# Optimization experiments

Measured on AMD Instinct MI355X. Metric: run time of the kernel, lower is better.

The kernel has to match this reference:

```python
import jax, jax.numpy as jnp
from jax import lax
import numpy as np

B, T, I, H = 4096, 200, 32, 6  # batch, seq_len, input_size, hidden


def _lstm_layer(x_seq, W_ih, W_hh, b_ih, b_hh):
    """Single unidirectional LSTM layer, PyTorch gate order (i,f,g,o).
    x_seq: [B,T,Din]. Returns (all_h [B,T,H], h_last [B,H])."""
    Bb = x_seq.shape[0]
    Hh = W_hh.shape[1]
    # Precompute input projections for all timesteps (hoisted out of the scan).
    x_proj = jnp.einsum('bti,gi->btg', x_seq, W_ih) + b_ih + b_hh  # [B,T,4H]

    def step(carry, xp_t):
        h, c = carry
        gates = xp_t + h @ W_hh.T  # [B,4H]
        i_g, f_g, g_g, o_g = jnp.split(gates, 4, axis=-1)
        i_g = jax.nn.sigmoid(i_g)
        f_g = jax.nn.sigmoid(f_g)
        g_g = jnp.tanh(g_g)
        o_g = jax.nn.sigmoid(o_g)
        c = f_g * c + i_g * g_g
        h = o_g * jnp.tanh(c)
        return (h, c), h

    init = (jnp.zeros((Bb, Hh), x_seq.dtype), jnp.zeros((Bb, Hh), x_seq.dtype))
    (h_last, _), hs = lax.scan(step, init, jnp.swapaxes(x_proj, 0, 1))  # time-major scan
    return jnp.swapaxes(hs, 0, 1), h_last


def setup_inputs() -> dict:
    key = jax.random.key(0)
    ks = jax.random.split(key, 11)
    s = 0.2  # ~ uniform(-1/sqrt(H)) scale for H=6
    inp = {
        'x': jax.random.normal(ks[0], (B, T, I), dtype=jnp.float32),
        'W_ih0': jax.random.normal(ks[1], (4 * H, I), dtype=jnp.float32) * s,
        'W_hh0': jax.random.normal(ks[2], (4 * H, H), dtype=jnp.float32) * s,
        'b_ih0': jax.random.normal(ks[3], (4 * H,), dtype=jnp.float32) * s,
        'b_hh0': jax.random.normal(ks[4], (4 * H,), dtype=jnp.float32) * s,
        'W_ih1': jax.random.normal(ks[5], (4 * H, H), dtype=jnp.float32) * s,
        'W_hh1': jax.random.normal(ks[6], (4 * H, H), dtype=jnp.float32) * s,
        'b_ih1': jax.random.normal(ks[7], (4 * H,), dtype=jnp.float32) * s,
        'b_hh1': jax.random.normal(ks[8], (4 * H,), dtype=jnp.float32) * s,
        'W_lin': jax.random.normal(ks[9], (1, H), dtype=jnp.float32) * s,
        'b_lin': jax.random.normal(ks[10], (1,), dtype=jnp.float32) * s,
    }
    return inp


def reference(x, W_ih0, W_hh0, b_ih0, b_hh0, W_ih1, W_hh1, b_ih1, b_hh1, W_lin, b_lin):
    # Layer 0 (eval mode: inter-layer dropout disabled)
    h1_seq, _ = _lstm_layer(x, W_ih0, W_hh0, b_ih0, b_hh0)
    # Layer 1
    _, h2_last = _lstm_layer(h1_seq, W_ih1, W_hh1, b_ih1, b_hh1)
    # Linear head on last layer's final hidden state: [B,1]
    return h2_last @ W_lin.T + b_lin
```

## Files before the change

### kernel.cpp

```cpp
#include <hip/hip_runtime.h>


#define BATCH 4096
#define TLEN  200
#define ISZ   32
#define HSZ   6
#define GSZ   24
#define TCH   64
#define XPITCH 28
#define XROWS (TCH + 1)

__device__ __forceinline__ float fast_sig(float x) {
    return __builtin_amdgcn_rcpf(1.0f + __expf(-x));
}
__device__ __forceinline__ float rl(float v, int l) {
    return __int_as_float(__builtin_amdgcn_readlane(__float_as_int(v), l));
}
template <int CTRL>
__device__ __forceinline__ float qperm(float v) {
    return __int_as_float(__builtin_amdgcn_mov_dpp(__float_as_int(v), CTRL, 0xf, 0xf, true));
}

__global__ void __launch_bounds__(64)
lstm_fused(
    const float* __restrict__ x,
    const float* __restrict__ Wih0, const float* __restrict__ Whh0,
    const float* __restrict__ bih0, const float* __restrict__ bhh0,
    const float* __restrict__ Wih1, const float* __restrict__ Whh1,
    const float* __restrict__ bih1, const float* __restrict__ bhh1,
    const float* __restrict__ Wlin, const float* __restrict__ blin,
    float* __restrict__ out)
{
    __shared__ __align__(16) float xp_lds[XROWS * XPITCH];

    const int lane = threadIdx.x;
    const int b    = blockIdx.x;

    const bool loHalf = (lane < 32);
    const int  p  = lane & 3;
    const int  jq = (lane & 31) >> 2;
    const int  j  = (jq < HSZ) ? jq : 0;
    const int  r  = 6 * p + j;

    float WA[HSZ], WB[HSZ];
    float base1 = 0.0f;
#pragma unroll
    for (int k = 0; k < HSZ; ++k) { WA[k] = 0.0f; WB[k] = 0.0f; }
    if (loHalf) {
#pragma unroll
        for (int k = 0; k < HSZ; ++k) WA[k] = Whh0[r * HSZ + k];
    } else {
#pragma unroll
        for (int k = 0; k < HSZ; ++k) { WA[k] = Wih1[r * HSZ + k]; WB[k] = Whh1[r * HSZ + k]; }
        base1 = bih1[r] + bhh1[r];
    }
    const float mg  = (p == 2) ? 2.0f : 1.0f;
    const float sg  = (p == 2) ? 2.0f : 1.0f;
    const float tgc = (p == 2) ? -1.0f : 0.0f;

    float c = 0.0f, h = 0.0f;

    for (int t0 = 0; t0 < TLEN; t0 += TCH) {
        const int tcl = min(TCH, TLEN - t0);

        {
            const int tIdx = min(t0 + lane, TLEN - 1);
            const float4* xrow = (const float4*)(x + ((size_t)b * TLEN + tIdx) * ISZ);
#pragma unroll
            for (int grp = 0; grp < 3; ++grp) {
                float acc[8];
#pragma unroll
                for (int rr = 0; rr < 8; ++rr)
                    acc[rr] = bih0[grp * 8 + rr] + bhh0[grp * 8 + rr];
#pragma unroll
                for (int kh = 0; kh < 2; ++kh) {
                    float4 xr[4];
#pragma unroll
                    for (int q = 0; q < 4; ++q) xr[q] = xrow[4 * kh + q];
#pragma unroll
                    for (int rr = 0; rr < 8; ++rr) {
                        const float4* wrow =
                            (const float4*)(Wih0 + (grp * 8 + rr) * ISZ + kh * 16);
#pragma unroll
                        for (int q = 0; q < 4; ++q) {
                            float4 w = wrow[q];
                            acc[rr] += w.x * xr[q].x + w.y * xr[q].y
                                     + w.z * xr[q].z + w.w * xr[q].w;
                        }
                    }
                }
                *(float4*)&xp_lds[lane * XPITCH + 8 * grp] =
                    make_float4(acc[0], acc[1], acc[2], acc[3]);
                *(float4*)&xp_lds[lane * XPITCH + 8 * grp + 4] =
                    make_float4(acc[4], acc[5], acc[6], acc[7]);
            }
        }

        const bool lastChunk = (t0 + TCH >= TLEN);
        const int  iters = tcl + (lastChunk ? 1 : 0);
        float xp_cur = xp_lds[r];
        int   it0 = 0;

        if (t0 == 0) {
            const float g  = loHalf ? xp_cur : base1;
            const float a  = fmaf(sg, fast_sig(mg * g), tgc);
            const float iq = qperm<0x00>(a);
            const float gq = qperm<0xAA>(a);
            const float oq = qperm<0xFF>(a);
            const float cn = iq * gq;
            const float th = fmaf(2.0f, fast_sig(2.0f * cn), -1.0f);
            const float hn = oq * th;
            c = loHalf ? cn : 0.0f;
            h = loHalf ? hn : 0.0f;
            xp_cur = xp_lds[XPITCH + r];
            it0 = 1;
        }

        for (int it = it0; it < iters; ++it) {
            const float h10 = rl(h, 0),  h11 = rl(h, 4),  h12 = rl(h, 8);
            const float h13 = rl(h, 12), h14 = rl(h, 16), h15 = rl(h, 20);
            const float h20 = rl(h, 32), h21 = rl(h, 36), h22 = rl(h, 40);
            const float h23 = rl(h, 44), h24 = rl(h, 48), h25 = rl(h, 52);

            const float xp_nxt = xp_lds[(it + 1) * XPITCH + r];

            const float g0 = loHalf ? xp_cur : base1;
            float a0 = fmaf(WA[0], h10, fmaf(WA[2], h12, fmaf(WA[4], h14, g0)));
            float a1 = fmaf(WA[1], h11, fmaf(WA[3], h13, WA[5] * h15));
            float b0 = fmaf(WB[0], h20, fmaf(WB[2], h22, WB[4] * h24));
            float b1 = fmaf(WB[1], h21, fmaf(WB[3], h23, WB[5] * h25));
            const float g = (a0 + a1) + (b0 + b1);
            const float a = fmaf(sg, fast_sig(mg * g), tgc);

            const float iq = qperm<0x00>(a);
            const float fq = qperm<0x55>(a);
            const float gq = qperm<0xAA>(a);
            const float oq = qperm<0xFF>(a);

            c = fmaf(fq, c, iq * gq);
            const float th = fmaf(2.0f, fast_sig(2.0f * c), -1.0f);
            h = oq * th;

            xp_cur = xp_nxt;
        }
    }

    float s = blin[0];
#pragma unroll
    for (int k = 0; k < HSZ; ++k) s = fmaf(Wlin[k], rl(h, 32 + 4 * k), s);
    if (lane == 0) out[b] = s;
}

extern "C" void kernel_launch(void* const* d_in, const int* in_sizes, int n_in,
                              void* d_out, int out_size, void* d_ws, size_t ws_size,
                              hipStream_t stream) {
    const float* x    = (const float*)d_in[0];
    const float* Wih0 = (const float*)d_in[1];
    const float* Whh0 = (const float*)d_in[2];
    const float* bih0 = (const float*)d_in[3];
    const float* bhh0 = (const float*)d_in[4];
    const float* Wih1 = (const float*)d_in[5];
    const float* Whh1 = (const float*)d_in[6];
    const float* bih1 = (const float*)d_in[7];
    const float* bhh1 = (const float*)d_in[8];
    const float* Wlin = (const float*)d_in[9];
    const float* blin = (const float*)d_in[10];
    float* out = (float*)d_out;

    lstm_fused<<<BATCH, 64, 0, stream>>>(x, Wih0, Whh0, bih0, bhh0,
                                         Wih1, Whh1, bih1, bhh1,
                                         Wlin, blin, out);
}
```

Measured before the change: 289.9 us.

## Split input projection into separate kernel and stream projections from global memory in scan

Moves the layer-0 input projection out of the fused LSTM kernel into its own grid-parallel kernel that writes a [B,208,24] workspace. The scan kernel then reads the precomputed projections directly from global memory with a two-step register prefetch, instead of computing 64-step chunks into LDS in between recurrent segments. This removes the serialized projection phases from the latency-bound recurrence, but adds a roughly 80 MB workspace round trip, a second launch, and global-load latency inside the scan loop. The old fused kernel is kept as a fallback when the workspace is too small.

```diff
diff --git a/kernel.cpp b/kernel.cpp
--- a/kernel.cpp
+++ b/kernel.cpp
@@ -6,20 +6,150 @@
 #define ISZ   32
 #define HSZ   6
 #define GSZ   24
+#define XPT   208
+#define XPB   (XPT * GSZ)
+
+__device__ __forceinline__ float fast_sig(float x) {
+    return __builtin_amdgcn_rcpf(1.0f + __expf(-x));
+}
+__device__ __forceinline__ float rl(float v, int l) {
+    return __int_as_float(__builtin_amdgcn_readlane(__float_as_int(v), l));
+}
+template <int CTRL>
+__device__ __forceinline__ float qperm(float v) {
+    return __int_as_float(__builtin_amdgcn_mov_dpp(__float_as_int(v), CTRL, 0xf, 0xf, true));
+}
+
+__global__ __launch_bounds__(64) void proj_kernel(
+    const float* __restrict__ x, const float* __restrict__ Wih0,
+    const float* __restrict__ bih0, const float* __restrict__ bhh0,
+    float* __restrict__ xp)
+{
+    const int lane = threadIdx.x;
+    const int t    = blockIdx.x * 64 + lane;
+    const int b    = blockIdx.y;
+    const int tc   = min(t, TLEN - 1);
+    const float4* xrow = (const float4*)(x + ((size_t)b * TLEN + tc) * ISZ);
+    float* orow = xp + (size_t)b * XPB + (size_t)tc * GSZ;
+
+#pragma unroll
+    for (int grp = 0; grp < 3; ++grp) {
+        float acc[8];
+#pragma unroll
+        for (int rr = 0; rr < 8; ++rr) acc[rr] = bih0[grp * 8 + rr] + bhh0[grp * 8 + rr];
+#pragma unroll
+        for (int kh = 0; kh < 2; ++kh) {
+            float4 xr[4];
+#pragma unroll
+            for (int q = 0; q < 4; ++q) xr[q] = xrow[4 * kh + q];
+#pragma unroll
+            for (int rr = 0; rr < 8; ++rr) {
+                const float4* wrow = (const float4*)(Wih0 + (grp * 8 + rr) * ISZ + kh * 16);
+#pragma unroll
+                for (int q = 0; q < 4; ++q) {
+                    float4 w = wrow[q];
+                    acc[rr] += w.x * xr[q].x + w.y * xr[q].y + w.z * xr[q].z + w.w * xr[q].w;
+                }
+            }
+        }
+        if (t < TLEN) {
+            *(float4*)&orow[8 * grp]     = make_float4(acc[0], acc[1], acc[2], acc[3]);
+            *(float4*)&orow[8 * grp + 4] = make_float4(acc[4], acc[5], acc[6], acc[7]);
+        }
+    }
+}
+
+__global__ __launch_bounds__(64) void scan_kernel(
+    const float* __restrict__ xp,
+    const float* __restrict__ Whh0,
+    const float* __restrict__ Wih1, const float* __restrict__ Whh1,
+    const float* __restrict__ bih1, const float* __restrict__ bhh1,
+    const float* __restrict__ Wlin, const float* __restrict__ blin,
+    float* __restrict__ out)
+{
+    const int lane = threadIdx.x;
+    const int b    = blockIdx.x;
+
+    const bool loHalf = (lane < 32);
+    const int  p  = lane & 3;
+    const int  jq = (lane & 31) >> 2;
+    const int  j  = (jq < HSZ) ? jq : 0;
+    const int  r  = 6 * p + j;
+
+    float WA[HSZ], WB[HSZ];
+    float base1 = 0.0f;
+#pragma unroll
+    for (int k = 0; k < HSZ; ++k) { WA[k] = 0.0f; WB[k] = 0.0f; }
+    if (loHalf) {
+#pragma unroll
+        for (int k = 0; k < HSZ; ++k) WA[k] = Whh0[r * HSZ + k];
+    } else {
+#pragma unroll
+        for (int k = 0; k < HSZ; ++k) { WA[k] = Wih1[r * HSZ + k]; WB[k] = Whh1[r * HSZ + k]; }
+        base1 = bih1[r] + bhh1[r];
+    }
+    const float mg  = (p == 2) ? 2.0f : 1.0f;
+    const float sg  = (p == 2) ? 2.0f : 1.0f;
+    const float tgc = (p == 2) ? -1.0f : 0.0f;
+
+    const float* xq = xp + (size_t)b * XPB + r;
+
+    float c = 0.0f, h = 0.0f;
+
+    float x0 = xq[0];
+    float x1 = xq[GSZ];
+    float x2 = xq[2 * GSZ];
+
+    {
+        const float g  = loHalf ? x0 : base1;
+        const float a  = fmaf(sg, fast_sig(mg * g), tgc);
+        const float iq = qperm<0x00>(a);
+        const float gq = qperm<0xAA>(a);
+        const float oq = qperm<0xFF>(a);
+        const float cn = iq * gq;
+        const float th = fmaf(2.0f, fast_sig(2.0f * cn), -1.0f);
+        const float hn = oq * th;
+        c = loHalf ? cn : 0.0f;
+        h = loHalf ? hn : 0.0f;
+    }
+
+    for (int it = 1; it <= TLEN; ++it) {
+        const float h10 = rl(h, 0),  h11 = rl(h, 4),  h12 = rl(h, 8);
+        const float h13 = rl(h, 12), h14 = rl(h, 16), h15 = rl(h, 20);
+        const float h20 = rl(h, 32), h21 = rl(h, 36), h22 = rl(h, 40);
+        const float h23 = rl(h, 44), h24 = rl(h, 48), h25 = rl(h, 52);
+
+        const float xnew = xq[(it + 2) * GSZ];
+
+        const float g0 = loHalf ? x1 : base1;
+        float a0 = fmaf(WA[0], h10, fmaf(WA[2], h12, fmaf(WA[4], h14, g0)));
+        float a1 = fmaf(WA[1], h11, fmaf(WA[3], h13, WA[5] * h15));
+        float b0 = fmaf(WB[0], h20, fmaf(WB[2], h22, WB[4] * h24));
+        float b1 = fmaf(WB[1], h21, fmaf(WB[3], h23, WB[5] * h25));
+        const float g = (a0 + a1) + (b0 + b1);
+        const float a = fmaf(sg, fast_sig(mg * g), tgc);
+
+        const float iq = qperm<0x00>(a);
+        const float fq = qperm<0x55>(a);
+        const float gq = qperm<0xAA>(a);
+        const float oq = qperm<0xFF>(a);
+
+        c = fmaf(fq, c, iq * gq);
+        const float th = fmaf(2.0f, fast_sig(2.0f * c), -1.0f);
+        h = oq * th;
+
+        x1 = x2; x2 = xnew;
+    }
+
+    float s = blin[0];
+#pragma unroll
+    for (int k = 0; k < HSZ; ++k) s = fmaf(Wlin[k], rl(h, 32 + 4 * k), s);
+    if (lane == 0) out[b] = s;
+}
+
 #define TCH   64
 #define XPITCH 28
 #define XROWS (TCH + 1)
-
-__device__ __forceinline__ float fast_sig(float x) {
-    return __builtin_amdgcn_rcpf(1.0f + __expf(-x));
-}
-__device__ __forceinline__ float rl(float v, int l) {
-    return __int_as_float(__builtin_amdgcn_readlane(__float_as_int(v), l));
-}
-template <int CTRL>
-__device__ __forceinline__ float qperm(float v) {
-    return __int_as_float(__builtin_amdgcn_mov_dpp(__float_as_int(v), CTRL, 0xf, 0xf, true));
-}
 
 __global__ void __launch_bounds__(64)
 lstm_fused(
@@ -62,7 +192,6 @@
 
     for (int t0 = 0; t0 < TLEN; t0 += TCH) {
         const int tcl = min(TCH, TLEN - t0);
-
         {
             const int tIdx = min(t0 + lane, TLEN - 1);
             const float4* xrow = (const float4*)(x + ((size_t)b * TLEN + tIdx) * ISZ);
@@ -167,7 +296,15 @@
     const float* blin = (const float*)d_in[10];
     float* out = (float*)d_out;
 
-    lstm_fused<<<BATCH, 64, 0, stream>>>(x, Wih0, Whh0, bih0, bhh0,
-                                         Wih1, Whh1, bih1, bhh1,
-                                         Wlin, blin, out);
-}
+    const size_t need = (size_t)BATCH * XPB * sizeof(float);
+    if (ws_size >= need) {
+        float* xp = (float*)d_ws;
+        proj_kernel<<<dim3(4, BATCH), 64, 0, stream>>>(x, Wih0, bih0, bhh0, xp);
+        scan_kernel<<<BATCH, 64, 0, stream>>>(xp, Whh0, Wih1, Whh1, bih1, bhh1,
+                                              Wlin, blin, out);
+    } else {
+        lstm_fused<<<BATCH, 64, 0, stream>>>(x, Wih0, Whh0, bih0, bhh0,
+                                             Wih1, Whh1, bih1, bhh1,
+                                             Wlin, blin, out);
+    }
+}
```

Result: slower. 336.6 us (+16.1%).

## Interleave layer-0 input projection with recurrent scan using an LDS ring buffer

Applied to the files above, without the earlier changes.

Replaces the chunked scheme, where each 64-step chunk first computed the input projection and then ran the serial recurrence, with a software pipeline. Small slices of the next window's x·W_ih0 projection are computed between scan steps and written into a 64-slot LDS ring. W_ih0 and the biases are staged once in LDS. The gate-g pre-scaling by 2 is folded into the weights, and launch bounds request 4 waves per SIMD. The goal is to hide the projection work in the latency gaps of the serial recurrence, at the cost of more register pressure and more complex indexing.

```diff
diff --git a/kernel.cpp b/kernel.cpp
--- a/kernel.cpp
+++ b/kernel.cpp
@@ -1,14 +1,14 @@
 #include <hip/hip_runtime.h>
 
 
-#define BATCH 4096
 #define TLEN  200
 #define ISZ   32
 #define HSZ   6
-#define GSZ   24
-#define TCH   64
-#define XPITCH 28
-#define XROWS (TCH + 1)
+#define RPITCH 25
+#define RING_DW (64 * RPITCH)
+#define WOFF  RING_DW
+#define BOFF  (WOFF + 768)
+#define LDS_DW (BOFF + 24)
 
 __device__ __forceinline__ float fast_sig(float x) {
     return __builtin_amdgcn_rcpf(1.0f + __expf(-x));
@@ -20,9 +20,11 @@
 __device__ __forceinline__ float qperm(float v) {
     return __int_as_float(__builtin_amdgcn_mov_dpp(__float_as_int(v), CTRL, 0xf, 0xf, true));
 }
-
-__global__ void __launch_bounds__(64)
-lstm_fused(
+__device__ __forceinline__ float dot4(float4 w, float4 v) {
+    return fmaf(w.x, v.x, fmaf(w.y, v.y, fmaf(w.z, v.z, w.w * v.w)));
+}
+
+__global__ __launch_bounds__(64, 4) void lstm_one(
     const float* __restrict__ x,
     const float* __restrict__ Wih0, const float* __restrict__ Whh0,
     const float* __restrict__ bih0, const float* __restrict__ bhh0,
@@ -31,10 +33,13 @@
     const float* __restrict__ Wlin, const float* __restrict__ blin,
     float* __restrict__ out)
 {
-    __shared__ __align__(16) float xp_lds[XROWS * XPITCH];
+    __shared__ float lds[LDS_DW];
 
     const int lane = threadIdx.x;
     const int b    = blockIdx.x;
+
+    const int o = lane & 1;
+    const int L = lane >> 1;
 
     const bool loHalf = (lane < 32);
     const int  p  = lane & 3;
@@ -42,113 +47,175 @@
     const int  j  = (jq < HSZ) ? jq : 0;
     const int  r  = 6 * p + j;
 
-    float WA[HSZ], WB[HSZ];
-    float base1 = 0.0f;
-#pragma unroll
-    for (int k = 0; k < HSZ; ++k) { WA[k] = 0.0f; WB[k] = 0.0f; }
+#define LDSW(ROW, KCQ) (*(const float4*)&lds[WOFF + ((o * 12 + (ROW)) << 5) + ((KCQ) << 2)])
+
+#pragma unroll
+    for (int k = 0; k < 13; ++k) {
+        const int idx = lane + (k << 6);
+        if (idx < 768)      lds[WOFF + idx] = Wih0[idx];
+        else if (idx < 792) lds[BOFF + idx - 768] = bih0[idx - 768] + bhh0[idx - 768];
+    }
+
+    float WA[6], WB[6], base1 = 0.0f, sgc = 1.0f, tgc = 0.0f;
+#pragma unroll
+    for (int k = 0; k < 6; ++k) { WA[k] = 0.0f; WB[k] = 0.0f; }
     if (loHalf) {
 #pragma unroll
-        for (int k = 0; k < HSZ; ++k) WA[k] = Whh0[r * HSZ + k];
+        for (int k = 0; k < 6; ++k) WA[k] = Whh0[r * 6 + k];
     } else {
 #pragma unroll
-        for (int k = 0; k < HSZ; ++k) { WA[k] = Wih1[r * HSZ + k]; WB[k] = Whh1[r * HSZ + k]; }
+        for (int k = 0; k < 6; ++k) { WA[k] = Wih1[r * 6 + k]; WB[k] = Whh1[r * 6 + k]; }
         base1 = bih1[r] + bhh1[r];
     }
-    const float mg  = (p == 2) ? 2.0f : 1.0f;
-    const float sg  = (p == 2) ? 2.0f : 1.0f;
-    const float tgc = (p == 2) ? -1.0f : 0.0f;
+    if (p == 2) {
+#pragma unroll
+        for (int k = 0; k < 6; ++k) { WA[k] *= 2.0f; WB[k] *= 2.0f; }
+        base1 *= 2.0f; sgc = 2.0f; tgc = -1.0f;
+    }
+
+    const float* xb = x + (size_t)b * TLEN * ISZ;
+
+#pragma unroll
+    for (int w01 = 0; w01 < 2; ++w01) {
+        const int t = (w01 << 5) + L;
+        const float4* xr4 = (const float4*)(xb + t * ISZ);
+        float4 xw[8];
+#pragma unroll
+        for (int q = 0; q < 8; ++q) xw[q] = xr4[q];
+        float a0c[12];
+#pragma unroll
+        for (int jj = 0; jj < 12; ++jj) a0c[jj] = 0.0f;
+#pragma unroll
+        for (int kc = 0; kc < 8; ++kc)
+#pragma unroll
+            for (int jj = 0; jj < 12; ++jj)
+                a0c[jj] += dot4(LDSW(jj, kc), xw[kc]);
+#pragma unroll
+        for (int jj = 0; jj < 12; ++jj) {
+            float v = a0c[jj] + lds[BOFF + o * 12 + jj];
+            if (jj < 6) v = (o == 1) ? v * 2.0f : v;
+            lds[t * RPITCH + o * 12 + jj] = v;
+        }
+    }
+
+    float acc[12];
+#pragma unroll
+    for (int jj = 0; jj < 12; ++jj) acc[jj] = 0.0f;
+    const float* pc = xb + (size_t)min(64 + L, TLEN - 1) * ISZ;
+    const float* pn = xb + (size_t)min(96 + L, TLEN - 1) * ISZ;
+    float4 f0, f1;
+    f1 = *((const float4*)pc);
+    float4 Wp0 = LDSW(0, 0), Wp1 = LDSW(1, 0), Wp2 = LDSW(2, 0);
 
     float c = 0.0f, h = 0.0f;
-
-    for (int t0 = 0; t0 < TLEN; t0 += TCH) {
-        const int tcl = min(TCH, TLEN - t0);
-
-        {
-            const int tIdx = min(t0 + lane, TLEN - 1);
-            const float4* xrow = (const float4*)(x + ((size_t)b * TLEN + tIdx) * ISZ);
-#pragma unroll
-            for (int grp = 0; grp < 3; ++grp) {
-                float acc[8];
-#pragma unroll
-                for (int rr = 0; rr < 8; ++rr)
-                    acc[rr] = bih0[grp * 8 + rr] + bhh0[grp * 8 + rr];
-#pragma unroll
-                for (int kh = 0; kh < 2; ++kh) {
-                    float4 xr[4];
-#pragma unroll
-                    for (int q = 0; q < 4; ++q) xr[q] = xrow[4 * kh + q];
-#pragma unroll
-                    for (int rr = 0; rr < 8; ++rr) {
-                        const float4* wrow =
-                            (const float4*)(Wih0 + (grp * 8 + rr) * ISZ + kh * 16);
-#pragma unroll
-                        for (int q = 0; q < 4; ++q) {
-                            float4 w = wrow[q];
-                            acc[rr] += w.x * xr[q].x + w.y * xr[q].y
-                                     + w.z * xr[q].z + w.w * xr[q].w;
-                        }
-                    }
-                }
-                *(float4*)&xp_lds[lane * XPITCH + 8 * grp] =
-                    make_float4(acc[0], acc[1], acc[2], acc[3]);
-                *(float4*)&xp_lds[lane * XPITCH + 8 * grp + 4] =
-                    make_float4(acc[4], acc[5], acc[6], acc[7]);
-            }
+    float xp_cur = lds[r];
+
+#define KC_HEAD(KC) do { \
+    f0 = f1; \
+    const float4* _srcp = ((KC) < 7) ? ((const float4*)pc + (KC) + 1) \
+                                     : ((const float4*)pn); \
+    f1 = *_srcp; \
+} while (0)
+
+#define SPREAD_STEP(RT, KC) do { \
+    acc[3*(RT)+0] += dot4(Wp0, f0); \
+    acc[3*(RT)+1] += dot4(Wp1, f0); \
+    acc[3*(RT)+2] += dot4(Wp2, f0); \
+    const int _rtn = ((RT) + 1) & 3; \
+    const int _kcn = ((RT) == 3) ? (((KC) + 1) & 7) : (KC); \
+    Wp0 = LDSW(3*_rtn + 0, _kcn); \
+    Wp1 = LDSW(3*_rtn + 1, _kcn); \
+    Wp2 = LDSW(3*_rtn + 2, _kcn); \
+} while (0)
+
+#define SCAN_STEP(ITV) do { \
+    const float h10=rl(h,0),  h11=rl(h,4),  h12=rl(h,8); \
+    const float h13=rl(h,12), h14=rl(h,16), h15=rl(h,20); \
+    const float h20=rl(h,32), h21=rl(h,36), h22=rl(h,40); \
+    const float h23=rl(h,44), h24=rl(h,48), h25=rl(h,52); \
+    const float _xn = lds[(((ITV) + 1) & 63) * RPITCH + r]; \
+    const float _g0 = loHalf ? xp_cur : base1; \
+    const float _a0 = fmaf(WA[0],h10, fmaf(WA[2],h12, fmaf(WA[4],h14, _g0))); \
+    const float _a1 = fmaf(WA[1],h11, fmaf(WA[3],h13, WA[5]*h15)); \
+    const float _b0 = fmaf(WB[0],h20, fmaf(WB[2],h22, WB[4]*h24)); \
+    const float _b1 = fmaf(WB[1],h21, fmaf(WB[3],h23, WB[5]*h25)); \
+    const float _g  = (_a0 + _a1) + (_b0 + _b1); \
+    const float _aG = fmaf(sgc, fast_sig(_g), tgc); \
+    const float _iq = qperm<0x00>(_aG), _fq = qperm<0x55>(_aG); \
+    const float _gq = qperm<0xAA>(_aG), _oq = qperm<0xFF>(_aG); \
+    c = fmaf(_fq, c, _iq * _gq); \
+    const float _th = fmaf(2.0f, fast_sig(2.0f * c), -1.0f); \
+    h = _oq * _th; \
+    xp_cur = _xn; \
+    if ((ITV) == 200) { \
+        float _s = blin[0]; \
+        _s = fmaf(Wlin[0], rl(h, 32), _s); \
+        _s = fmaf(Wlin[1], rl(h, 36), _s); \
+        _s = fmaf(Wlin[2], rl(h, 40), _s); \
+        _s = fmaf(Wlin[3], rl(h, 44), _s); \
+        _s = fmaf(Wlin[4], rl(h, 48), _s); \
+        _s = fmaf(Wlin[5], rl(h, 52), _s); \
+        if (lane == 0) out[b] = _s; \
+    } \
+} while (0)
+
+#define ENTRY(IT0) do { \
+    const int _slot = ((IT0) + 32 + L) & 63; \
+    _Pragma("unroll") \
+    for (int _jj = 0; _jj < 12; ++_jj) { \
+        float _v = acc[_jj] + lds[BOFF + o * 12 + _jj]; \
+        if (_jj < 6) _v = (o == 1) ? _v * 2.0f : _v; \
+        lds[_slot * RPITCH + o * 12 + _jj] = _v; \
+        acc[_jj] = 0.0f; \
+    } \
+    pc = pn; \
+    pn = xb + (size_t)min((IT0) + 96 + L, TLEN - 1) * ISZ; \
+} while (0)
+
+    KC_HEAD(0);
+    SPREAD_STEP(0, 0);
+    {
+        const float g  = loHalf ? xp_cur : base1;
+        const float aG = fmaf(sgc, fast_sig(g), tgc);
+        const float iq = qperm<0x00>(aG), gq = qperm<0xAA>(aG), oq = qperm<0xFF>(aG);
+        const float cn = iq * gq;
+        const float th = fmaf(2.0f, fast_sig(2.0f * cn), -1.0f);
+        c = loHalf ? cn : 0.0f;
+        h = loHalf ? (oq * th) : 0.0f;
+        xp_cur = lds[RPITCH + r];
+    }
+
+    SPREAD_STEP(1, 0); SCAN_STEP(1);
+    SPREAD_STEP(2, 0); SCAN_STEP(2);
+    SPREAD_STEP(3, 0); SCAN_STEP(3);
+    for (int kc = 1; kc < 8; ++kc) {
+        KC_HEAD(kc);
+        const int itb = kc << 2;
+        SPREAD_STEP(0, kc); SCAN_STEP(itb + 0);
+        SPREAD_STEP(1, kc); SCAN_STEP(itb + 1);
+        SPREAD_STEP(2, kc); SCAN_STEP(itb + 2);
+        SPREAD_STEP(3, kc); SCAN_STEP(itb + 3);
+    }
+
+    for (int w = 1; w < 7; ++w) {
+        const int it0 = w << 5;
+        ENTRY(it0);
+        for (int kc = 0; kc < 8; ++kc) {
+            const int itb = it0 + (kc << 2);
+            if (itb > 200) break;
+            KC_HEAD(kc);
+            SPREAD_STEP(0, kc); SCAN_STEP(itb + 0);
+            SPREAD_STEP(1, kc); SCAN_STEP(itb + 1);
+            SPREAD_STEP(2, kc); SCAN_STEP(itb + 2);
+            SPREAD_STEP(3, kc); SCAN_STEP(itb + 3);
         }
-
-        const bool lastChunk = (t0 + TCH >= TLEN);
-        const int  iters = tcl + (lastChunk ? 1 : 0);
-        float xp_cur = xp_lds[r];
-        int   it0 = 0;
-
-        if (t0 == 0) {
-            const float g  = loHalf ? xp_cur : base1;
-            const float a  = fmaf(sg, fast_sig(mg * g), tgc);
-            const float iq = qperm<0x00>(a);
-            const float gq = qperm<0xAA>(a);
-            const float oq = qperm<0xFF>(a);
-            const float cn = iq * gq;
-            const float th = fmaf(2.0f, fast_sig(2.0f * cn), -1.0f);
-            const float hn = oq * th;
-            c = loHalf ? cn : 0.0f;
-            h = loHalf ? hn : 0.0f;
-            xp_cur = xp_lds[XPITCH + r];
-            it0 = 1;
-        }
-
-        for (int it = it0; it < iters; ++it) {
-            const float h10 = rl(h, 0),  h11 = rl(h, 4),  h12 = rl(h, 8);
-            const float h13 = rl(h, 12), h14 = rl(h, 16), h15 = rl(h, 20);
-            const float h20 = rl(h, 32), h21 = rl(h, 36), h22 = rl(h, 40);
-            const float h23 = rl(h, 44), h24 = rl(h, 48), h25 = rl(h, 52);
-
-            const float xp_nxt = xp_lds[(it + 1) * XPITCH + r];
-
-            const float g0 = loHalf ? xp_cur : base1;
-            float a0 = fmaf(WA[0], h10, fmaf(WA[2], h12, fmaf(WA[4], h14, g0)));
-            float a1 = fmaf(WA[1], h11, fmaf(WA[3], h13, WA[5] * h15));
-            float b0 = fmaf(WB[0], h20, fmaf(WB[2], h22, WB[4] * h24));
-            float b1 = fmaf(WB[1], h21, fmaf(WB[3], h23, WB[5] * h25));
-            const float g = (a0 + a1) + (b0 + b1);
-            const float a = fmaf(sg, fast_sig(mg * g), tgc);
-
-            const float iq = qperm<0x00>(a);
-            const float fq = qperm<0x55>(a);
-            const float gq = qperm<0xAA>(a);
-            const float oq = qperm<0xFF>(a);
-
-            c = fmaf(fq, c, iq * gq);
-            const float th = fmaf(2.0f, fast_sig(2.0f * c), -1.0f);
-            h = oq * th;
-
-            xp_cur = xp_nxt;
-        }
-    }
-
-    float s = blin[0];
-#pragma unroll
-    for (int k = 0; k < HSZ; ++k) s = fmaf(Wlin[k], rl(h, 32 + 4 * k), s);
-    if (lane == 0) out[b] = s;
+    }
+
+#undef LDSW
+#undef KC_HEAD
+#undef SPREAD_STEP
+#undef SCAN_STEP
+#undef ENTRY
 }
 
 extern "C" void kernel_launch(void* const* d_in, const int* in_sizes, int n_in,
@@ -167,7 +234,7 @@
     const float* blin = (const float*)d_in[10];
     float* out = (float*)d_out;
 
-    lstm_fused<<<BATCH, 64, 0, stream>>>(x, Wih0, Whh0, bih0, bhh0,
-                                         Wih1, Whh1, bih1, bhh1,
-                                         Wlin, blin, out);
-}
+    lstm_one<<<4096, 64, 0, stream>>>(x, Wih0, Whh0, bih0, bhh0,
+                                      Wih1, Whh1, bih1, bhh1,
+                                      Wlin, blin, out);
+}
```

After: 257.1 us. 11.3% less time.
